# Performance work log

Measured on AMD Instinct MI355X. Metric: run time of the kernel, lower is better.

The kernel has to match this reference:

```python
import jax, jax.numpy as jnp
import numpy as np

IN_FEATURES = 512
NUM_TREES = 512
DEPTH = 5
NLEAF = 2 ** DEPTH
RESPONSE_DIM = 1
BATCH = 2048


def make_path_map():
    # OBLIVIOUS_map from DeTree.InitPathWay: nodes[j] = j (oblivious tree),
    # index 2*node + bit into the flattened [depth, 2] choice tensor.
    path = []
    for no in range(NLEAF):
        b = no
        for j in range(DEPTH):
            path.append(2 * j + (b % 2))
            b //= 2
    return np.asarray(path, dtype=np.int32)  # [NLEAF * DEPTH]


def setup_inputs() -> dict:
    key = jax.random.key(0)
    k1, k2, k3, k4, k5 = jax.random.split(key, 5)
    x = jax.random.normal(k1, (BATCH, IN_FEATURES), dtype=jnp.float32)
    # nn.init.uniform_ on [in_features, num_trees * depth]
    feat_attention = jax.random.uniform(k2, (IN_FEATURES, NUM_TREES * DEPTH), dtype=jnp.float32)
    feature_thresholds = jax.random.normal(k3, (NUM_TREES, DEPTH), dtype=jnp.float32)
    log_temperatures = jax.random.normal(k4, (NUM_TREES, DEPTH), dtype=jnp.float32) * 0.1
    response = jax.random.normal(k5, (NUM_TREES, RESPONSE_DIM, NLEAF), dtype=jnp.float32)
    path_map = jnp.asarray(make_path_map())
    return {"x": x, "feat_attention": feat_attention,
            "feature_thresholds": feature_thresholds,
            "log_temperatures": log_temperatures,
            "response": response, "path_map": path_map}


def reference(x, feat_attention, feature_thresholds, log_temperatures, response, path_map):
    B, F = x.shape
    n, d = feature_thresholds.shape
    # feature gating: softmax over the feature axis (dim=0)
    choice_weight = jax.nn.softmax(feat_attention, axis=0).reshape(F, n, d)
    feature_values = jnp.einsum('bf,fnd->bnd', x, choice_weight)  # [B, n, d]
    # temperature-scaled split logits
    tl = (feature_values - feature_thresholds) * jnp.exp(-log_temperatures)
    logits = jnp.stack([-tl, tl], axis=-1)  # [B, n, d, 2]
    # sparsemoid binary gate
    choice = jnp.clip(0.5 * logits + 0.5, 0.0, 1.0)
    # route through tree paths: gather per-leaf path gates, product along depth
    gate = choice.reshape(B, n, d * 2)[:, :, path_map].reshape(B, n, -1, d)
    bins_prob = jnp.prod(gate, axis=-1)  # [B, n, nLeaf]
    out = jnp.einsum('bnl,ncl->bnc', bins_prob, response)  # [B, n, response_dim]
    return out.reshape(B, -1)  # flatten_output=True
```

## Files before the change

kernel.cpp:

```cpp
#include <hip/hip_runtime.h>
#include <hip/hip_bf16.h>

#define F_DIM 512
#define NT 512
#define DEPTH 5
#define NCOL (NT * DEPTH)
#define BATCH 2048

typedef __attribute__((ext_vector_type(8))) short bf16x8;
typedef __attribute__((ext_vector_type(4))) float f32x4;

__device__ __forceinline__ void gl2lds16(const void* g, void* l) {
    __builtin_amdgcn_global_load_lds((const __attribute__((address_space(1))) void*)g,
                                     (__attribute__((address_space(3))) void*)l,
                                     16, 0, 0);
}

__global__ __launch_bounds__(512) void prep(const float* __restrict__ x,
                                            const float* __restrict__ fa,
                                            __hip_bfloat16* __restrict__ Xb,
                                            __hip_bfloat16* __restrict__ Wt) {
    if (blockIdx.x >= 80) {
        const size_t i = (size_t)(blockIdx.x - 80) * 512 + threadIdx.x;
        const float4 v = ((const float4*)x)[i];
        union { ushort4 u; __hip_bfloat16 h[4]; } pk;
        pk.h[0] = __float2bfloat16(v.x);
        pk.h[1] = __float2bfloat16(v.y);
        pk.h[2] = __float2bfloat16(v.z);
        pk.h[3] = __float2bfloat16(v.w);
        ((ushort4*)Xb)[i] = pk.u;
        return;
    }
    const int l = threadIdx.x & 31;
    const int g = threadIdx.x >> 5;
    const int col = blockIdx.x * 32 + l;
    const int f0 = g * 32;
    __shared__ float red[16][32];

    float e[32];
    float s = 0.f;
#pragma unroll
    for (int i = 0; i < 32; ++i) {
        e[i] = __expf(fa[(size_t)(f0 + i) * NCOL + col]);
        s += e[i];
    }
    red[g][l] = s;
    __syncthreads();

    float S = 0.f;
#pragma unroll
    for (int gg = 0; gg < 16; ++gg) S += red[gg][l];
    const float inv = 1.0f / S;

    __hip_bfloat16* dst = Wt + (size_t)col * F_DIM + f0;
#pragma unroll
    for (int i = 0; i < 32; i += 8) {
        union { uint4 u; __hip_bfloat16 h[8]; } pk;
#pragma unroll
        for (int jj = 0; jj < 8; ++jj)
            pk.h[jj] = __float2bfloat16(e[i + jj] * inv);
        *(uint4*)(dst + i) = pk.u;
    }
}

__global__ __launch_bounds__(256, 2) void gemm_tree(const __hip_bfloat16* __restrict__ A,
                                                    const __hip_bfloat16* __restrict__ Bt,
                                                    const float* __restrict__ th,
                                                    const float* __restrict__ lt,
                                                    const float* __restrict__ resp,
                                                    float* __restrict__ out) {
    __shared__ __align__(16) char smem[57344];

    const int tid = threadIdx.x;
    const int w = tid >> 6;
    const int l = tid & 63;
    const int m0 = blockIdx.y * 64;
    const int n0c = blockIdx.x * 160;
    const int n0t = blockIdx.x * 32;
    const int wm = (w & 1) * 32;
    const int wn = (w >> 1) * 80;

    f32x4 acc[2][5] = {};

    const int srow = l >> 3;
    const int schunk = (l & 7) ^ srow;

    auto stage = [&](int kt, int buf) {
        const int k0 = kt * 64;
        char* base = smem + buf * 28672;
#pragma unroll
        for (int q = 0; q < 2; ++q) {
            const int g = q * 4 + w;
            gl2lds16(A + ((size_t)(m0 + g * 8 + srow) * F_DIM + k0 + schunk * 8),
                     base + g * 8 * 64 * 2);
        }
#pragma unroll
        for (int q = 0; q < 5; ++q) {
            const int g = q * 4 + w;
            gl2lds16(Bt + ((size_t)(n0c + g * 8 + srow) * F_DIM + k0 + schunk * 8),
                     base + 8192 + g * 8 * 64 * 2);
        }
    };

    stage(0, 0);
#pragma unroll
    for (int kt = 0; kt < 8; ++kt) {
        const int cur = kt & 1;
        __builtin_amdgcn_sched_barrier(0);
        if (kt < 7) {
            stage(kt + 1, cur ^ 1);
            asm volatile("s_waitcnt vmcnt(7)" ::: "memory");
        } else {
            asm volatile("s_waitcnt vmcnt(0)" ::: "memory");
        }
        __builtin_amdgcn_s_barrier();
        __builtin_amdgcn_sched_barrier(0);

        const __hip_bfloat16* As = (const __hip_bfloat16*)(smem + cur * 28672);
        const __hip_bfloat16* Bs = As + 4096;
#pragma unroll
        for (int ks = 0; ks < 2; ++ks) {
            const int cb = ks * 4 + (l >> 4);
            bf16x8 af[2], bfr[5];
#pragma unroll
            for (int im = 0; im < 2; ++im) {
                const int r = wm + im * 16 + (l & 15);
                af[im] = *(const bf16x8*)(As + r * 64 + ((cb ^ (r & 7)) * 8));
            }
#pragma unroll
            for (int in = 0; in < 5; ++in) {
                const int r = wn + in * 16 + (l & 15);
                bfr[in] = *(const bf16x8*)(Bs + r * 64 + ((cb ^ (r & 7)) * 8));
            }
#pragma unroll
            for (int im = 0; im < 2; ++im)
#pragma unroll
                for (int in = 0; in < 5; ++in)
                    acc[im][in] = __builtin_amdgcn_mfma_f32_16x16x32_bf16(
                        af[im], bfr[in], acc[im][in], 0, 0, 0);
        }
        __builtin_amdgcn_sched_barrier(0);
        __builtin_amdgcn_s_barrier();
    }
    __builtin_amdgcn_sched_barrier(0);

    float* E = (float*)smem;
    const int tree = tid & 31;
    const int rg = tid >> 5;
    const int gt = n0t + tree;

    float al[DEPTH], be[DEPTH];
#pragma unroll
    for (int j = 0; j < DEPTH; ++j) {
        const float a = 0.5f * __expf(-lt[gt * DEPTH + j]);
        al[j] = a;
        be[j] = 0.5f - th[gt * DEPTH + j] * a;
    }
    float rs[32];
#pragma unroll
    for (int i = 0; i < 32; ++i) rs[i] = resp[gt * 32 + i];

    const int PAD = 161;
#pragma unroll
    for (int im = 0; im < 2; ++im) {
#pragma unroll
        for (int in = 0; in < 5; ++in) {
            const int scol = wn + in * 16 + (l & 15);
#pragma unroll
            for (int r = 0; r < 4; ++r) {
                const int sr = (w & 1) * 16 + (l >> 4) * 4 + r;
                E[sr * PAD + scol] = acc[im][in][r];
            }
        }
        __syncthreads();

#pragma unroll
        for (int rr = 0; rr < 4; ++rr) {
            const int s = rg * 4 + rr;
            const int gb = m0 + ((s < 16) ? (im * 16 + s) : (32 + im * 16 + (s - 16)));
            const float* f = E + s * PAD + tree * 5;
            float c1[DEPTH];
#pragma unroll
            for (int j = 0; j < DEPTH; ++j) {
                const float v = fmaf(al[j], f[j], be[j]);
                c1[j] = fminf(fmaxf(v, 0.f), 1.f);
            }
            float s16[16], s8[8], s4[4], s2[2];
#pragma unroll
            for (int m = 0; m < 16; ++m) s16[m] = fmaf(c1[0], rs[2*m+1] - rs[2*m], rs[2*m]);
#pragma unroll
            for (int m = 0; m < 8; ++m)  s8[m]  = fmaf(c1[1], s16[2*m+1] - s16[2*m], s16[2*m]);
#pragma unroll
            for (int m = 0; m < 4; ++m)  s4[m]  = fmaf(c1[2], s8[2*m+1] - s8[2*m], s8[2*m]);
#pragma unroll
            for (int m = 0; m < 2; ++m)  s2[m]  = fmaf(c1[3], s4[2*m+1] - s4[2*m], s4[2*m]);
            out[(size_t)gb * NT + gt] = fmaf(c1[4], s2[1] - s2[0], s2[0]);
        }
        __syncthreads();
    }
}

extern "C" void kernel_launch(void* const* d_in, const int* in_sizes, int n_in,
                              void* d_out, int out_size, void* d_ws, size_t ws_size,
                              hipStream_t stream) {
    const float* x    = (const float*)d_in[0];
    const float* fa   = (const float*)d_in[1];
    const float* th   = (const float*)d_in[2];
    const float* lt   = (const float*)d_in[3];
    const float* resp = (const float*)d_in[4];

    char* ws = (char*)d_ws;
    __hip_bfloat16* Wt = (__hip_bfloat16*)(ws);
    __hip_bfloat16* Xb = (__hip_bfloat16*)(ws + (4u << 20));
    float* out = (float*)d_out;

    hipLaunchKernelGGL(prep, dim3(80 + 512), dim3(512), 0, stream, x, fa, Xb, Wt);
    hipLaunchKernelGGL(gemm_tree, dim3(NCOL / 160, BATCH / 64), dim3(256), 0, stream,
                       Xb, Wt, th, lt, resp, out);
}
```

Measured before the change: 82.14 us.

## Fuse fp32-to-bf16 conversion of x into GEMM A-tile staging

Removes the separate x-to-bf16 conversion from the prep kernel. The GEMM now loads fp32 x straight into registers, converts it, and writes swizzled bf16 A tiles to LDS, with the B tile still loaded asynchronously. This drops a 2 MB bf16 intermediate write and read plus 512 prep blocks. In exchange, each GEMM block rereads fp32 x (twice the bytes across 16 column blocks), and there is an extra barrier and register-staged path per k-step.

```diff
diff --git a/kernel.cpp b/kernel.cpp
--- a/kernel.cpp
+++ b/kernel.cpp
@@ -16,21 +16,17 @@
                                      16, 0, 0);
 }
 
-__global__ __launch_bounds__(512) void prep(const float* __restrict__ x,
-                                            const float* __restrict__ fa,
-                                            __hip_bfloat16* __restrict__ Xb,
+__device__ __forceinline__ bf16x8 pack8(float4 a, float4 b) {
+    union { bf16x8 v; __hip_bfloat16 h[8]; } u;
+    u.h[0] = __float2bfloat16(a.x); u.h[1] = __float2bfloat16(a.y);
+    u.h[2] = __float2bfloat16(a.z); u.h[3] = __float2bfloat16(a.w);
+    u.h[4] = __float2bfloat16(b.x); u.h[5] = __float2bfloat16(b.y);
+    u.h[6] = __float2bfloat16(b.z); u.h[7] = __float2bfloat16(b.w);
+    return u.v;
+}
+
+__global__ __launch_bounds__(512) void prep(const float* __restrict__ fa,
                                             __hip_bfloat16* __restrict__ Wt) {
-    if (blockIdx.x >= 80) {
-        const size_t i = (size_t)(blockIdx.x - 80) * 512 + threadIdx.x;
-        const float4 v = ((const float4*)x)[i];
-        union { ushort4 u; __hip_bfloat16 h[4]; } pk;
-        pk.h[0] = __float2bfloat16(v.x);
-        pk.h[1] = __float2bfloat16(v.y);
-        pk.h[2] = __float2bfloat16(v.z);
-        pk.h[3] = __float2bfloat16(v.w);
-        ((ushort4*)Xb)[i] = pk.u;
-        return;
-    }
     const int l = threadIdx.x & 31;
     const int g = threadIdx.x >> 5;
     const int col = blockIdx.x * 32 + l;
@@ -63,7 +59,7 @@
     }
 }
 
-__global__ __launch_bounds__(256, 2) void gemm_tree(const __hip_bfloat16* __restrict__ A,
+__global__ __launch_bounds__(256, 2) void gemm_tree(const float* __restrict__ x,
                                                     const __hip_bfloat16* __restrict__ Bt,
                                                     const float* __restrict__ th,
                                                     const float* __restrict__ lt,
@@ -85,37 +81,34 @@
     const int srow = l >> 3;
     const int schunk = (l & 7) ^ srow;
 
-    auto stage = [&](int kt, int buf) {
+    const int ar = tid >> 2;
+    const int ac = (tid & 3) * 2;
+
+    float4 av0, av1, av2, av3;
+
+    auto a_load = [&](int kt) {
+        const float* p = x + (size_t)(m0 + ar) * F_DIM + kt * 64 + ac * 8;
+        av0 = ((const float4*)p)[0];
+        av1 = ((const float4*)p)[1];
+        av2 = ((const float4*)p)[2];
+        av3 = ((const float4*)p)[3];
+    };
+    auto a_write = [&](int buf) {
+        __hip_bfloat16* As = (__hip_bfloat16*)(smem + buf * 28672);
+        *(bf16x8*)(As + ar * 64 + ((ac ^ (ar & 7)) * 8))       = pack8(av0, av1);
+        *(bf16x8*)(As + ar * 64 + (((ac + 1) ^ (ar & 7)) * 8)) = pack8(av2, av3);
+    };
+    auto stageB = [&](int kt, int buf) {
         const int k0 = kt * 64;
-        char* base = smem + buf * 28672;
-#pragma unroll
-        for (int q = 0; q < 2; ++q) {
-            const int g = q * 4 + w;
-            gl2lds16(A + ((size_t)(m0 + g * 8 + srow) * F_DIM + k0 + schunk * 8),
-                     base + g * 8 * 64 * 2);
-        }
+        char* base = smem + buf * 28672 + 8192;
 #pragma unroll
         for (int q = 0; q < 5; ++q) {
             const int g = q * 4 + w;
             gl2lds16(Bt + ((size_t)(n0c + g * 8 + srow) * F_DIM + k0 + schunk * 8),
-                     base + 8192 + g * 8 * 64 * 2);
-        }
-    };
-
-    stage(0, 0);
-#pragma unroll
-    for (int kt = 0; kt < 8; ++kt) {
-        const int cur = kt & 1;
-        __builtin_amdgcn_sched_barrier(0);
-        if (kt < 7) {
-            stage(kt + 1, cur ^ 1);
-            asm volatile("s_waitcnt vmcnt(7)" ::: "memory");
-        } else {
-            asm volatile("s_waitcnt vmcnt(0)" ::: "memory");
-        }
-        __builtin_amdgcn_s_barrier();
-        __builtin_amdgcn_sched_barrier(0);
-
+                     base + g * 8 * 64 * 2);
+        }
+    };
+    auto compute = [&](int cur) {
         const __hip_bfloat16* As = (const __hip_bfloat16*)(smem + cur * 28672);
         const __hip_bfloat16* Bs = As + 4096;
 #pragma unroll
@@ -139,8 +132,42 @@
                     acc[im][in] = __builtin_amdgcn_mfma_f32_16x16x32_bf16(
                         af[im], bfr[in], acc[im][in], 0, 0, 0);
         }
+    };
+
+    a_load(0);
+    __builtin_amdgcn_sched_barrier(0);
+    stageB(0, 0);
+    __builtin_amdgcn_sched_barrier(0);
+    asm volatile("s_waitcnt vmcnt(5)" ::: "memory");
+    a_write(0);
+    asm volatile("s_waitcnt lgkmcnt(0)" ::: "memory");
+    __builtin_amdgcn_sched_barrier(0);
+
+#pragma unroll
+    for (int kt = 0; kt < 8; ++kt) {
+        const int cur = kt & 1;
+        if (kt < 7) {
+            a_load(kt + 1);
+            __builtin_amdgcn_sched_barrier(0);
+            stageB(kt + 1, cur ^ 1);
+            __builtin_amdgcn_sched_barrier(0);
+            asm volatile("s_waitcnt vmcnt(9)" ::: "memory");
+        } else {
+            asm volatile("s_waitcnt vmcnt(0)" ::: "memory");
+        }
+        __builtin_amdgcn_s_barrier();
         __builtin_amdgcn_sched_barrier(0);
-        __builtin_amdgcn_s_barrier();
+
+        compute(cur);
+        __builtin_amdgcn_sched_barrier(0);
+
+        if (kt < 7) {
+            asm volatile("s_waitcnt vmcnt(5)" ::: "memory");
+            a_write(cur ^ 1);
+            asm volatile("s_waitcnt lgkmcnt(0)" ::: "memory");
+            __builtin_amdgcn_sched_barrier(0);
+            __builtin_amdgcn_s_barrier();
+        }
     }
     __builtin_amdgcn_sched_barrier(0);
 
@@ -211,10 +238,9 @@
 
     char* ws = (char*)d_ws;
     __hip_bfloat16* Wt = (__hip_bfloat16*)(ws);
-    __hip_bfloat16* Xb = (__hip_bfloat16*)(ws + (4u << 20));
     float* out = (float*)d_out;
 
-    hipLaunchKernelGGL(prep, dim3(80 + 512), dim3(512), 0, stream, x, fa, Xb, Wt);
+    hipLaunchKernelGGL(prep, dim3(80), dim3(512), 0, stream, fa, Wt);
     hipLaunchKernelGGL(gemm_tree, dim3(NCOL / 160, BATCH / 64), dim3(256), 0, stream,
-                       Xb, Wt, th, lt, resp, out);
-}
+                       x, Wt, th, lt, resp, out);
+}
```

New measurement: 87.41 us. 6.4% more time.
